# Kernel tuning notes

Measured on AMD Instinct MI355X. Metric: run time of the kernel, lower is better.

## Reference

```python
import jax, jax.numpy as jnp
import numpy as np

B = 64      # graphs per batch
N = 1024    # nodes per graph (equal-size graphs -> static top-k)
D = 256     # in_dim
DEG = 16    # avg degree
K = 512     # k = ratio * N, ratio = 0.5
E = B * N * DEG
NT = B * N


def setup_inputs() -> dict:
    key = jax.random.key(0)
    ks = jax.random.split(key, 8)
    feature = jax.random.normal(ks[0], (NT, D), jnp.float32)
    gid = jnp.repeat(jnp.arange(B), N * DEG)          # graph id per edge
    src = gid * N + jax.random.randint(ks[1], (E,), 0, N)
    dst = gid * N + jax.random.randint(ks[2], (E,), 0, N)
    label = jax.random.randint(ks[3], (B,), 0, 2)
    W = jax.random.normal(ks[4], (D, 1), jnp.float32) / np.sqrt(D)   # GraphConv weight
    b = jnp.zeros((1,), jnp.float32)                                  # GraphConv bias
    lin1_w = jax.random.normal(ks[5], (2, 1), jnp.float32) / np.sqrt(2.0)
    lin1_b = jnp.zeros((1,), jnp.float32)
    return dict(feature=feature, src=src, dst=dst, label=label,
                W=W, b=b, lin1_w=lin1_w, lin1_b=lin1_b)


def reference(feature, src, dst, label, W, b, lin1_w, lin1_b):
    fdt = feature.dtype
    # ---- get_bias_score: distance-to-class-center score ----
    node_label = jnp.repeat(label, N).astype(fdt)                 # [NT]
    gemb = feature.reshape(B, N, D).mean(axis=1)                  # AvgPooling per graph [B, D]
    lab_f = label.astype(fdt)                                     # [B]
    n1 = jnp.maximum(lab_f.sum(), 1.0)
    n0 = jnp.maximum((1.0 - lab_f).sum(), 1.0)
    center0 = (gemb * (1.0 - lab_f)[:, None]).sum(0) / n0         # [D]
    center1 = (gemb * lab_f[:, None]).sum(0) / n1                 # [D]
    d0 = jnp.sqrt(((feature - center0) ** 2).sum(-1))             # [NT]
    d1 = jnp.sqrt(((feature - center1) ** 2).sum(-1))             # [NT]
    score_distance = (d0 - d1) * ((node_label - 0.5) * 2.0)       # [NT]
    # ---- GraphConv(in_dim, 1), norm='both' (DGL semantics) ----
    ones_e = jnp.ones((E,), fdt)
    deg_out = jax.ops.segment_sum(ones_e, src, NT)
    deg_in = jax.ops.segment_sum(ones_e, dst, NT)
    ns = jnp.maximum(deg_out, 1.0) ** -0.5                        # src-side norm
    nd = jnp.maximum(deg_in, 1.0) ** -0.5                         # dst-side norm
    h = (feature @ W) * ns[:, None]                               # project first (out<in) [NT,1]
    agg = jax.ops.segment_sum(h[src], dst, NT)                    # [NT,1]
    score_gcn = (agg * nd[:, None] + b)[:, 0]                     # [NT]
    # ---- combine two scores with lin1: Linear(2, 1) ----
    score = jnp.stack([score_gcn, score_distance], axis=-1) @ lin1_w + lin1_b  # [NT,1]
    sflat = score[:, 0]
    # ---- per-graph top-k (mytopk with equal-size graphs -> static k) ----
    _, idx = jax.lax.top_k(sflat.reshape(B, N), K)                # [B,K] local indices
    perm = (idx + (jnp.arange(B) * N)[:, None]).reshape(-1)       # [B*K] global indices
    mask = jnp.ones((NT,), bool).at[perm].set(False)
    perm_com = jnp.nonzero(mask, size=NT - B * K)[0]              # complement, static size
    # ---- gather + tanh-gated features ----
    feature_dis = feature[perm] * jnp.tanh(sflat[perm])[:, None]          # [B*K, D]
    feature_com = feature[perm_com] * jnp.tanh(sflat[perm_com])[:, None]  # [B*(N-K), D]
    score_soft = jax.nn.softmax(score, axis=0)                    # softmax over all nodes
    return feature_dis, feature_com, perm, perm_com, score_soft
```

## Files before the change

### kernel.cpp

```cpp
#include <hip/hip_runtime.h>
#include <math.h>

#define Bg   64
#define Nn   1024
#define Dd   256
#define EPG  16384
#define NT   (Bg * Nn)
#define Kk   512

#define OFF_DIS   0
#define OFF_COM   8388608
#define OFF_PERM  16777216
#define OFF_PCOM  16809984
#define OFF_SOFT  16842752

#define WS_H0     0
#define WS_SFLAT  (NT * 4)
#define WS_GPART  (NT * 4 * 2)
#define WS_REDM   (WS_GPART + 1024 * 256 * 4)
#define WS_REDS   (WS_REDM + 256)
#define WS_C0     (WS_REDS + 256)
#define WS_C1     (WS_C0 + 1024)
#define WS_PERMI  (WS_C1 + 1024)
#define WS_PCOMI  (WS_PERMI + 32768 * 4)
#define WS_SGCN   (WS_PCOMI + 32768 * 4)

__global__ __launch_bounds__(256) void k_col(
        const float* __restrict__ f, const float* __restrict__ W,
        float* __restrict__ gpart, float* __restrict__ h0) {
    __shared__ float4 scol4[1024];
    int blk = blockIdx.x, t = threadIdx.x;
    int gid = t >> 4, sub = t & 15;
    int base = blk * 64 + gid * 4;
    const float4* f4 = (const float4*)f;
    const float4* W4 = (const float4*)W;
    float4 w[4];
    #pragma unroll
    for (int it = 0; it < 4; ++it) w[it] = W4[it * 16 + sub];
    float4 cs[4];
    #pragma unroll
    for (int it = 0; it < 4; ++it) cs[it] = make_float4(0.f, 0.f, 0.f, 0.f);
    float4 v[4][4];
    #pragma unroll
    for (int k = 0; k < 4; ++k) {
        size_t bofs = (size_t)(base + k) * 64;
        #pragma unroll
        for (int it = 0; it < 4; ++it) v[k][it] = f4[bofs + it * 16 + sub];
    }
    #pragma unroll
    for (int k = 0; k < 4; ++k) {
        float d = 0.f;
        #pragma unroll
        for (int it = 0; it < 4; ++it) {
            cs[it].x += v[k][it].x; cs[it].y += v[k][it].y;
            cs[it].z += v[k][it].z; cs[it].w += v[k][it].w;
            d += v[k][it].x * w[it].x + v[k][it].y * w[it].y
               + v[k][it].z * w[it].z + v[k][it].w * w[it].w;
        }
        #pragma unroll
        for (int o = 1; o < 16; o <<= 1) d += __shfl_xor(d, o);
        if (sub == 0) h0[base + k] = d;
    }
    #pragma unroll
    for (int it = 0; it < 4; ++it) scol4[gid * 64 + it * 16 + sub] = cs[it];
    __syncthreads();
    if (t < 64) {
        float4 s = make_float4(0.f, 0.f, 0.f, 0.f);
        #pragma unroll
        for (int g2 = 0; g2 < 16; ++g2) {
            float4 u = scol4[g2 * 64 + t];
            s.x += u.x; s.y += u.y; s.z += u.z; s.w += u.w;
        }
        ((float4*)(gpart + blk * Dd))[t] = s;
    }
}

__global__ __launch_bounds__(1024) void k_edge(
        const int* __restrict__ src, const int* __restrict__ dst,
        const int* __restrict__ label, const float* __restrict__ h0,
        const float* __restrict__ gpart, const float* __restrict__ b,
        float* __restrict__ sgcn, float* __restrict__ c0, float* __restrict__ c1) {
    __shared__ uint4 ep4[4096];
    __shared__ int   sdo[1024];
    __shared__ int   sdi[1024];
    __shared__ float shn[1024];
    __shared__ float ssc[1024];
    __shared__ float sc0[1024];
    __shared__ float sc1[1024];

    int g = blockIdx.x, t = threadIdx.x;
    sdo[t] = 0; sdi[t] = 0;

    if (g == 0) {
        int col = t & 255, chunk = t >> 8;
        float a0 = 0.f, a1 = 0.f;
        for (int gg = chunk * 16; gg < chunk * 16 + 16; ++gg) {
            float v = 0.f;
            #pragma unroll
            for (int p = 0; p < 16; ++p) v += gpart[(gg * 16 + p) * Dd + col];
            if (label[gg]) a1 += v; else a0 += v;
        }
        sc0[t] = a0; sc1[t] = a1;
        __syncthreads();
        if (t < Dd) {
            int n1 = 0;
            for (int gg = 0; gg < Bg; ++gg) n1 += label[gg];
            float fn1 = fmaxf((float)n1, 1.f);
            float fn0 = fmaxf((float)(Bg - n1), 1.f);
            float s0 = sc0[t] + sc0[256 + t] + sc0[512 + t] + sc0[768 + t];
            float s1 = sc1[t] + sc1[256 + t] + sc1[512 + t] + sc1[768 + t];
            c0[t] = s0 * (1.f / (float)Nn) / fn0;
            c1[t] = s1 * (1.f / (float)Nn) / fn1;
        }
    }
    __syncthreads();

    {
        const int4* s4 = (const int4*)(src + g * EPG);
        const int4* d4 = (const int4*)(dst + g * EPG);
        #pragma unroll
        for (int i = t; i < EPG / 4; i += 1024) {
            int4 ss = s4[i];
            int4 dd = d4[i];
            int s0 = ss.x & (Nn - 1), s1 = ss.y & (Nn - 1), s2 = ss.z & (Nn - 1), s3 = ss.w & (Nn - 1);
            int e0 = dd.x & (Nn - 1), e1 = dd.y & (Nn - 1), e2 = dd.z & (Nn - 1), e3 = dd.w & (Nn - 1);
            uint4 pk;
            pk.x = (unsigned)(s0 | (e0 << 16));
            pk.y = (unsigned)(s1 | (e1 << 16));
            pk.z = (unsigned)(s2 | (e2 << 16));
            pk.w = (unsigned)(s3 | (e3 << 16));
            ep4[i] = pk;
            atomicAdd(&sdo[s0], 1); atomicAdd(&sdo[s1], 1);
            atomicAdd(&sdo[s2], 1); atomicAdd(&sdo[s3], 1);
            atomicAdd(&sdi[e0], 1); atomicAdd(&sdi[e1], 1);
            atomicAdd(&sdi[e2], 1); atomicAdd(&sdi[e3], 1);
        }
    }
    __syncthreads();

    {
        int dg = sdo[t]; if (dg < 1) dg = 1;
        shn[t] = h0[g * Nn + t] / sqrtf((float)dg);
        ssc[t] = 0.f;
    }
    __syncthreads();

    #pragma unroll
    for (int i = t; i < EPG / 4; i += 1024) {
        uint4 pk = ep4[i];
        atomicAdd(&ssc[pk.x >> 16], shn[pk.x & 0xFFFF]);
        atomicAdd(&ssc[pk.y >> 16], shn[pk.y & 0xFFFF]);
        atomicAdd(&ssc[pk.z >> 16], shn[pk.z & 0xFFFF]);
        atomicAdd(&ssc[pk.w >> 16], shn[pk.w & 0xFFFF]);
    }
    __syncthreads();

    {
        int dg = sdi[t]; if (dg < 1) dg = 1;
        sgcn[g * Nn + t] = ssc[t] / sqrtf((float)dg) + b[0];
    }
}

__global__ __launch_bounds__(256) void k_score(
        const float* __restrict__ f, const float* __restrict__ c0,
        const float* __restrict__ c1, const float* __restrict__ sgcn,
        const int* __restrict__ label, const float* __restrict__ lw,
        const float* __restrict__ lb, float* __restrict__ sflat) {
    int t = threadIdx.x;
    int gid = t >> 4, sub = t & 15;
    int row0 = blockIdx.x * 32 + gid * 2;
    int g = row0 >> 10;
    const float4* f4 = (const float4*)f;
    float4 c0r[4], c1r[4];
    #pragma unroll
    for (int it = 0; it < 4; ++it) {
        c0r[it] = ((const float4*)c0)[it * 16 + sub];
        c1r[it] = ((const float4*)c1)[it * 16 + sub];
    }
    float sgn = label[g] ? 1.f : -1.f;
    float lw0 = lw[0], lw1 = lw[1], lb0 = lb[0];
    float4 v[2][4];
    #pragma unroll
    for (int r = 0; r < 2; ++r) {
        size_t bofs = (size_t)(row0 + r) * 64;
        #pragma unroll
        for (int it = 0; it < 4; ++it) v[r][it] = f4[bofs + it * 16 + sub];
    }
    #pragma unroll
    for (int r = 0; r < 2; ++r) {
        float a0 = 0.f, a1 = 0.f;
        #pragma unroll
        for (int it = 0; it < 4; ++it) {
            float dx;
            dx = v[r][it].x - c0r[it].x; a0 += dx * dx;
            dx = v[r][it].y - c0r[it].y; a0 += dx * dx;
            dx = v[r][it].z - c0r[it].z; a0 += dx * dx;
            dx = v[r][it].w - c0r[it].w; a0 += dx * dx;
            dx = v[r][it].x - c1r[it].x; a1 += dx * dx;
            dx = v[r][it].y - c1r[it].y; a1 += dx * dx;
            dx = v[r][it].z - c1r[it].z; a1 += dx * dx;
            dx = v[r][it].w - c1r[it].w; a1 += dx * dx;
        }
        #pragma unroll
        for (int o = 1; o < 16; o <<= 1) {
            a0 += __shfl_xor(a0, o);
            a1 += __shfl_xor(a1, o);
        }
        if (sub == 0) {
            int row = row0 + r;
            float sdist = (sqrtf(a0) - sqrtf(a1)) * sgn;
            sflat[row] = sgcn[row] * lw0 + sdist * lw1 + lb0;
        }
    }
}

__global__ __launch_bounds__(512) void k_topk(
        const float* __restrict__ sflat, int* __restrict__ permI,
        int* __restrict__ pcomI, float* __restrict__ out,
        float* __restrict__ redM, float* __restrict__ redS) {
    __shared__ unsigned long long sk[1024];
    __shared__ int   sflag[1024];
    __shared__ int   swave[8];
    __shared__ float sred[16];
    int g = blockIdx.x, t = threadIdx.x;
    int lane = t & 63, w = t >> 6;
    float v0 = sflat[g * Nn + t];
    float v1 = sflat[g * Nn + t + 512];
    unsigned u0 = __float_as_uint(v0);
    unsigned u1 = __float_as_uint(v1);
    unsigned o0 = u0 ^ ((u0 >> 31) ? 0xFFFFFFFFu : 0x80000000u);
    unsigned o1 = u1 ^ ((u1 >> 31) ? 0xFFFFFFFFu : 0x80000000u);
    sk[t]       = ((unsigned long long)o0 << 32) | (unsigned)(1023 - t);
    sk[t + 512] = ((unsigned long long)o1 << 32) | (unsigned)(1023 - (t + 512));
    __syncthreads();
    for (int k = 2; k <= 1024; k <<= 1) {
        for (int j = k >> 1; j > 0; j >>= 1) {
            int l = ((t & ~(j - 1)) << 1) | (t & (j - 1));
            int r = l | j;
            unsigned long long a = sk[l], bk = sk[r];
            bool up = ((l & k) == 0);
            if ((a < bk) == up) { sk[l] = bk; sk[r] = a; }
            __syncthreads();
        }
    }
    sflag[t] = 1; sflag[t + 512] = 1;
    __syncthreads();
    {
        int loc = 1023 - (int)(sk[t] & 0xFFFFFFFFu);
        sflag[loc] = 0;
        int gi = g * Nn + loc;
        permI[g * Kk + t] = gi;
        out[OFF_PERM + g * Kk + t] = (float)gi;
    }
    __syncthreads();
    int f0 = sflag[2 * t], f1 = sflag[2 * t + 1];
    int f2 = f0 + f1;
    int inc = f2;
    for (int o = 1; o < 64; o <<= 1) {
        int y = __shfl_up(inc, o);
        if (lane >= o) inc += y;
    }
    if (lane == 63) swave[w] = inc;
    __syncthreads();
    if (t < 8) {
        int a = swave[t];
        for (int o = 1; o < 8; o <<= 1) {
            int y = __shfl_up(a, o);
            if (t >= o) a += y;
        }
        swave[t] = a;
    }
    __syncthreads();
    int basep = ((w > 0) ? swave[w - 1] : 0) + (inc - f2);
    if (f0) {
        int gi = g * Nn + 2 * t;
        pcomI[g * Kk + basep] = gi;
        out[OFF_PCOM + g * Kk + basep] = (float)gi;
    }
    if (f1) {
        int pos = basep + f0;
        int gi = g * Nn + 2 * t + 1;
        pcomI[g * Kk + pos] = gi;
        out[OFF_PCOM + g * Kk + pos] = (float)gi;
    }
    float m = fmaxf(v0, v1);
    for (int o = 32; o > 0; o >>= 1) m = fmaxf(m, __shfl_xor(m, o));
    if (lane == 0) sred[w] = m;
    __syncthreads();
    if (t < 8) {
        float a = sred[t];
        for (int o = 4; o > 0; o >>= 1) a = fmaxf(a, __shfl_xor(a, o));
        if (t == 0) sred[0] = a;
    }
    __syncthreads();
    m = sred[0];
    float s = expf(v0 - m) + expf(v1 - m);
    for (int o = 32; o > 0; o >>= 1) s += __shfl_xor(s, o);
    if (lane == 0) sred[8 + w] = s;
    __syncthreads();
    if (t < 8) {
        float a = sred[8 + t];
        for (int o = 4; o > 0; o >>= 1) a += __shfl_xor(a, o);
        if (t == 0) { redM[g] = m; redS[g] = a; }
    }
}

__global__ __launch_bounds__(256) void k_write(
        const float* __restrict__ f, const int* __restrict__ permI,
        const int* __restrict__ pcomI, const float* __restrict__ sflat,
        const float* __restrict__ redM, const float* __restrict__ redS,
        float* __restrict__ out) {
    __shared__ float sMS[2];
    int t = threadIdx.x;
    if (t < 64) {
        float m = redM[t];
        float mm = m;
        for (int o = 32; o > 0; o >>= 1) mm = fmaxf(mm, __shfl_xor(mm, o));
        float s = redS[t] * expf(m - mm);
        for (int o = 32; o > 0; o >>= 1) s += __shfl_xor(s, o);
        if (t == 0) { sMS[0] = mm; sMS[1] = s; }
    }
    __syncthreads();
    float M = sMS[0], S = sMS[1];
    if (t < 32) {
        int i = blockIdx.x * 32 + t;
        out[OFF_SOFT + i] = expf(sflat[i] - M) / S;
    }
    int w = t >> 6, lane = t & 63;
    int j0 = blockIdx.x * 32 + w * 8;
    int rows[8];
    float tv[8];
    #pragma unroll
    for (int i = 0; i < 8; ++i) {
        int j = j0 + i;
        rows[i] = (j < 32768) ? permI[j] : pcomI[j - 32768];
    }
    #pragma unroll
    for (int i = 0; i < 8; ++i) tv[i] = sflat[rows[i]];
    #pragma unroll
    for (int i = 0; i < 8; ++i) tv[i] = tanhf(tv[i]);
    const float4* f4 = (const float4*)f;
    float4* o4 = (float4*)out;
    float4 v[8];
    #pragma unroll
    for (int i = 0; i < 8; ++i) v[i] = f4[(size_t)rows[i] * 64 + lane];
    #pragma unroll
    for (int i = 0; i < 8; ++i) {
        o4[(size_t)(j0 + i) * 64 + lane] =
            make_float4(v[i].x * tv[i], v[i].y * tv[i], v[i].z * tv[i], v[i].w * tv[i]);
    }
}

extern "C" void kernel_launch(void* const* d_in, const int* in_sizes, int n_in,
                              void* d_out, int out_size, void* d_ws, size_t ws_size,
                              hipStream_t stream) {
    const float* feature = (const float*)d_in[0];
    const int*   src     = (const int*)d_in[1];
    const int*   dst     = (const int*)d_in[2];
    const int*   label   = (const int*)d_in[3];
    const float* W       = (const float*)d_in[4];
    const float* b       = (const float*)d_in[5];
    const float* lw      = (const float*)d_in[6];
    const float* lb      = (const float*)d_in[7];
    float* out = (float*)d_out;
    char*  ws  = (char*)d_ws;

    float* h0    = (float*)(ws + WS_H0);
    float* sflat = (float*)(ws + WS_SFLAT);
    float* gpart = (float*)(ws + WS_GPART);
    float* redM  = (float*)(ws + WS_REDM);
    float* redS  = (float*)(ws + WS_REDS);
    float* c0    = (float*)(ws + WS_C0);
    float* c1    = (float*)(ws + WS_C1);
    int*   permI = (int*)(ws + WS_PERMI);
    int*   pcomI = (int*)(ws + WS_PCOMI);
    float* sgcn  = (float*)(ws + WS_SGCN);

    k_col  <<<1024, 256,  0, stream>>>(feature, W, gpart, h0);
    k_edge <<<Bg,   1024, 0, stream>>>(src, dst, label, h0, gpart, b, sgcn, c0, c1);
    k_score<<<2048, 256,  0, stream>>>(feature, c0, c1, sgcn, label, lw, lb, sflat);
    k_topk <<<Bg,   512,  0, stream>>>(sflat, permI, pcomI, out, redM, redS);
    k_write<<<2048, 256,  0, stream>>>(feature, permI, pcomI, sflat, redM, redS, out);
}
```

Before: 199.4 us.

## Overlap edge degree counting with feature column pass in one launch

The edge packing and degree histogram work now runs in 64 extra blocks of the feature column-sum/projection kernel, so it overlaps with the bandwidth-bound feature pass. The packed edges and degrees go to workspace, and a second kernel does only the scatter-add aggregation. The class-center reduction moves from block 0 into a separate 65th block, so it no longer serialises ahead of one graph's edge work. This adds global writes and reads of about 4 MB of packed edges and the degree arrays, and it uses 256-thread blocks for the histogram instead of 1024.

```diff
diff --git a/kernel.cpp b/kernel.cpp
--- a/kernel.cpp
+++ b/kernel.cpp
@@ -24,74 +24,133 @@
 #define WS_PERMI  (WS_C1 + 1024)
 #define WS_PCOMI  (WS_PERMI + 32768 * 4)
 #define WS_SGCN   (WS_PCOMI + 32768 * 4)
-
-__global__ __launch_bounds__(256) void k_col(
+#define WS_EPACK  (WS_SGCN + NT * 4)
+#define WS_DO     (WS_EPACK + Bg * EPG * 4)
+#define WS_DI     (WS_DO + NT * 4)
+
+__global__ __launch_bounds__(256) void k_mix(
         const float* __restrict__ f, const float* __restrict__ W,
-        float* __restrict__ gpart, float* __restrict__ h0) {
-    __shared__ float4 scol4[1024];
+        const int* __restrict__ src, const int* __restrict__ dst,
+        float* __restrict__ gpart, float* __restrict__ h0,
+        unsigned* __restrict__ epack, int* __restrict__ dout,
+        int* __restrict__ dinn) {
+    __shared__ alignas(16) char smem[16384];
     int blk = blockIdx.x, t = threadIdx.x;
-    int gid = t >> 4, sub = t & 15;
-    int base = blk * 64 + gid * 4;
-    const float4* f4 = (const float4*)f;
-    const float4* W4 = (const float4*)W;
-    float4 w[4];
-    #pragma unroll
-    for (int it = 0; it < 4; ++it) w[it] = W4[it * 16 + sub];
-    float4 cs[4];
-    #pragma unroll
-    for (int it = 0; it < 4; ++it) cs[it] = make_float4(0.f, 0.f, 0.f, 0.f);
-    float4 v[4][4];
-    #pragma unroll
-    for (int k = 0; k < 4; ++k) {
-        size_t bofs = (size_t)(base + k) * 64;
-        #pragma unroll
-        for (int it = 0; it < 4; ++it) v[k][it] = f4[bofs + it * 16 + sub];
-    }
-    #pragma unroll
-    for (int k = 0; k < 4; ++k) {
-        float d = 0.f;
-        #pragma unroll
-        for (int it = 0; it < 4; ++it) {
-            cs[it].x += v[k][it].x; cs[it].y += v[k][it].y;
-            cs[it].z += v[k][it].z; cs[it].w += v[k][it].w;
-            d += v[k][it].x * w[it].x + v[k][it].y * w[it].y
-               + v[k][it].z * w[it].z + v[k][it].w * w[it].w;
-        }
-        #pragma unroll
-        for (int o = 1; o < 16; o <<= 1) d += __shfl_xor(d, o);
-        if (sub == 0) h0[base + k] = d;
-    }
-    #pragma unroll
-    for (int it = 0; it < 4; ++it) scol4[gid * 64 + it * 16 + sub] = cs[it];
-    __syncthreads();
-    if (t < 64) {
-        float4 s = make_float4(0.f, 0.f, 0.f, 0.f);
-        #pragma unroll
-        for (int g2 = 0; g2 < 16; ++g2) {
-            float4 u = scol4[g2 * 64 + t];
-            s.x += u.x; s.y += u.y; s.z += u.z; s.w += u.w;
-        }
-        ((float4*)(gpart + blk * Dd))[t] = s;
-    }
-}
-
-__global__ __launch_bounds__(1024) void k_edge(
-        const int* __restrict__ src, const int* __restrict__ dst,
-        const int* __restrict__ label, const float* __restrict__ h0,
-        const float* __restrict__ gpart, const float* __restrict__ b,
-        float* __restrict__ sgcn, float* __restrict__ c0, float* __restrict__ c1) {
-    __shared__ uint4 ep4[4096];
-    __shared__ int   sdo[1024];
-    __shared__ int   sdi[1024];
+    if (blk < 1024) {
+        float4* scol4 = (float4*)smem;
+        int gid = t >> 4, sub = t & 15;
+        int base = blk * 64 + gid * 4;
+        const float4* f4 = (const float4*)f;
+        const float4* W4 = (const float4*)W;
+        float4 w[4];
+        #pragma unroll
+        for (int it = 0; it < 4; ++it) w[it] = W4[it * 16 + sub];
+        float4 cs[4];
+        #pragma unroll
+        for (int it = 0; it < 4; ++it) cs[it] = make_float4(0.f, 0.f, 0.f, 0.f);
+        float4 v[4][4];
+        #pragma unroll
+        for (int k = 0; k < 4; ++k) {
+            size_t bofs = (size_t)(base + k) * 64;
+            #pragma unroll
+            for (int it = 0; it < 4; ++it) v[k][it] = f4[bofs + it * 16 + sub];
+        }
+        #pragma unroll
+        for (int k = 0; k < 4; ++k) {
+            float d = 0.f;
+            #pragma unroll
+            for (int it = 0; it < 4; ++it) {
+                cs[it].x += v[k][it].x; cs[it].y += v[k][it].y;
+                cs[it].z += v[k][it].z; cs[it].w += v[k][it].w;
+                d += v[k][it].x * w[it].x + v[k][it].y * w[it].y
+                   + v[k][it].z * w[it].z + v[k][it].w * w[it].w;
+            }
+            #pragma unroll
+            for (int o = 1; o < 16; o <<= 1) d += __shfl_xor(d, o);
+            if (sub == 0) h0[base + k] = d;
+        }
+        #pragma unroll
+        for (int it = 0; it < 4; ++it) scol4[gid * 64 + it * 16 + sub] = cs[it];
+        __syncthreads();
+        if (t < 64) {
+            float4 s = make_float4(0.f, 0.f, 0.f, 0.f);
+            #pragma unroll
+            for (int g2 = 0; g2 < 16; ++g2) {
+                float4 u = scol4[g2 * 64 + t];
+                s.x += u.x; s.y += u.y; s.z += u.z; s.w += u.w;
+            }
+            ((float4*)(gpart + blk * Dd))[t] = s;
+        }
+    } else {
+        int* sdo = (int*)smem;
+        int* sdi = (int*)(smem + 4096);
+        int g = blk - 1024;
+        #pragma unroll
+        for (int j = 0; j < 4; ++j) { sdo[t + j * 256] = 0; sdi[t + j * 256] = 0; }
+        __syncthreads();
+        const int4* s4 = (const int4*)(src + g * EPG);
+        const int4* d4 = (const int4*)(dst + g * EPG);
+        uint4* p4 = (uint4*)(epack + g * EPG);
+        #pragma unroll
+        for (int i = t; i < EPG / 4; i += 256) {
+            int4 ss = s4[i];
+            int4 dd = d4[i];
+            int s0 = ss.x & (Nn - 1), s1 = ss.y & (Nn - 1), s2 = ss.z & (Nn - 1), s3 = ss.w & (Nn - 1);
+            int e0 = dd.x & (Nn - 1), e1 = dd.y & (Nn - 1), e2 = dd.z & (Nn - 1), e3 = dd.w & (Nn - 1);
+            uint4 pk;
+            pk.x = (unsigned)(s0 | (e0 << 16));
+            pk.y = (unsigned)(s1 | (e1 << 16));
+            pk.z = (unsigned)(s2 | (e2 << 16));
+            pk.w = (unsigned)(s3 | (e3 << 16));
+            p4[i] = pk;
+            atomicAdd(&sdo[s0], 1); atomicAdd(&sdo[s1], 1);
+            atomicAdd(&sdo[s2], 1); atomicAdd(&sdo[s3], 1);
+            atomicAdd(&sdi[e0], 1); atomicAdd(&sdi[e1], 1);
+            atomicAdd(&sdi[e2], 1); atomicAdd(&sdi[e3], 1);
+        }
+        __syncthreads();
+        #pragma unroll
+        for (int j = 0; j < 4; ++j) {
+            dout[g * Nn + t + j * 256] = sdo[t + j * 256];
+            dinn[g * Nn + t + j * 256] = sdi[t + j * 256];
+        }
+    }
+}
+
+__global__ __launch_bounds__(1024) void k_edge2(
+        const unsigned* __restrict__ epack, const int* __restrict__ dout,
+        const int* __restrict__ dinn, const int* __restrict__ label,
+        const float* __restrict__ h0, const float* __restrict__ gpart,
+        const float* __restrict__ b, float* __restrict__ sgcn,
+        float* __restrict__ c0, float* __restrict__ c1) {
     __shared__ float shn[1024];
     __shared__ float ssc[1024];
     __shared__ float sc0[1024];
     __shared__ float sc1[1024];
-
-    int g = blockIdx.x, t = threadIdx.x;
-    sdo[t] = 0; sdi[t] = 0;
-
-    if (g == 0) {
+    int blk = blockIdx.x, t = threadIdx.x;
+    if (blk < 64) {
+        int g = blk;
+        {
+            int dg = dout[g * Nn + t]; if (dg < 1) dg = 1;
+            shn[t] = h0[g * Nn + t] / sqrtf((float)dg);
+            ssc[t] = 0.f;
+        }
+        __syncthreads();
+        const uint4* p4 = (const uint4*)(epack + g * EPG);
+        #pragma unroll
+        for (int i = t; i < EPG / 4; i += 1024) {
+            uint4 pk = p4[i];
+            atomicAdd(&ssc[pk.x >> 16], shn[pk.x & 0xFFFF]);
+            atomicAdd(&ssc[pk.y >> 16], shn[pk.y & 0xFFFF]);
+            atomicAdd(&ssc[pk.z >> 16], shn[pk.z & 0xFFFF]);
+            atomicAdd(&ssc[pk.w >> 16], shn[pk.w & 0xFFFF]);
+        }
+        __syncthreads();
+        {
+            int dg = dinn[g * Nn + t]; if (dg < 1) dg = 1;
+            sgcn[g * Nn + t] = ssc[t] / sqrtf((float)dg) + b[0];
+        }
+    } else {
         int col = t & 255, chunk = t >> 8;
         float a0 = 0.f, a1 = 0.f;
         for (int gg = chunk * 16; gg < chunk * 16 + 16; ++gg) {
@@ -112,52 +171,6 @@
             c0[t] = s0 * (1.f / (float)Nn) / fn0;
             c1[t] = s1 * (1.f / (float)Nn) / fn1;
         }
-    }
-    __syncthreads();
-
-    {
-        const int4* s4 = (const int4*)(src + g * EPG);
-        const int4* d4 = (const int4*)(dst + g * EPG);
-        #pragma unroll
-        for (int i = t; i < EPG / 4; i += 1024) {
-            int4 ss = s4[i];
-            int4 dd = d4[i];
-            int s0 = ss.x & (Nn - 1), s1 = ss.y & (Nn - 1), s2 = ss.z & (Nn - 1), s3 = ss.w & (Nn - 1);
-            int e0 = dd.x & (Nn - 1), e1 = dd.y & (Nn - 1), e2 = dd.z & (Nn - 1), e3 = dd.w & (Nn - 1);
-            uint4 pk;
-            pk.x = (unsigned)(s0 | (e0 << 16));
-            pk.y = (unsigned)(s1 | (e1 << 16));
-            pk.z = (unsigned)(s2 | (e2 << 16));
-            pk.w = (unsigned)(s3 | (e3 << 16));
-            ep4[i] = pk;
-            atomicAdd(&sdo[s0], 1); atomicAdd(&sdo[s1], 1);
-            atomicAdd(&sdo[s2], 1); atomicAdd(&sdo[s3], 1);
-            atomicAdd(&sdi[e0], 1); atomicAdd(&sdi[e1], 1);
-            atomicAdd(&sdi[e2], 1); atomicAdd(&sdi[e3], 1);
-        }
-    }
-    __syncthreads();
-
-    {
-        int dg = sdo[t]; if (dg < 1) dg = 1;
-        shn[t] = h0[g * Nn + t] / sqrtf((float)dg);
-        ssc[t] = 0.f;
-    }
-    __syncthreads();
-
-    #pragma unroll
-    for (int i = t; i < EPG / 4; i += 1024) {
-        uint4 pk = ep4[i];
-        atomicAdd(&ssc[pk.x >> 16], shn[pk.x & 0xFFFF]);
-        atomicAdd(&ssc[pk.y >> 16], shn[pk.y & 0xFFFF]);
-        atomicAdd(&ssc[pk.z >> 16], shn[pk.z & 0xFFFF]);
-        atomicAdd(&ssc[pk.w >> 16], shn[pk.w & 0xFFFF]);
-    }
-    __syncthreads();
-
-    {
-        int dg = sdi[t]; if (dg < 1) dg = 1;
-        sgcn[g * Nn + t] = ssc[t] / sqrtf((float)dg) + b[0];
     }
 }
 
@@ -365,19 +378,22 @@
     float* out = (float*)d_out;
     char*  ws  = (char*)d_ws;
 
-    float* h0    = (float*)(ws + WS_H0);
-    float* sflat = (float*)(ws + WS_SFLAT);
-    float* gpart = (float*)(ws + WS_GPART);
-    float* redM  = (float*)(ws + WS_REDM);
-    float* redS  = (float*)(ws + WS_REDS);
-    float* c0    = (float*)(ws + WS_C0);
-    float* c1    = (float*)(ws + WS_C1);
-    int*   permI = (int*)(ws + WS_PERMI);
-    int*   pcomI = (int*)(ws + WS_PCOMI);
-    float* sgcn  = (float*)(ws + WS_SGCN);
-
-    k_col  <<<1024, 256,  0, stream>>>(feature, W, gpart, h0);
-    k_edge <<<Bg,   1024, 0, stream>>>(src, dst, label, h0, gpart, b, sgcn, c0, c1);
+    float*    h0    = (float*)(ws + WS_H0);
+    float*    sflat = (float*)(ws + WS_SFLAT);
+    float*    gpart = (float*)(ws + WS_GPART);
+    float*    redM  = (float*)(ws + WS_REDM);
+    float*    redS  = (float*)(ws + WS_REDS);
+    float*    c0    = (float*)(ws + WS_C0);
+    float*    c1    = (float*)(ws + WS_C1);
+    int*      permI = (int*)(ws + WS_PERMI);
+    int*      pcomI = (int*)(ws + WS_PCOMI);
+    float*    sgcn  = (float*)(ws + WS_SGCN);
+    unsigned* epack = (unsigned*)(ws + WS_EPACK);
+    int*      dout  = (int*)(ws + WS_DO);
+    int*      dinn  = (int*)(ws + WS_DI);
+
+    k_mix  <<<1088, 256,  0, stream>>>(feature, W, src, dst, gpart, h0, epack, dout, dinn);
+    k_edge2<<<65,   1024, 0, stream>>>(epack, dout, dinn, label, h0, gpart, b, sgcn, c0, c1);
     k_score<<<2048, 256,  0, stream>>>(feature, c0, c1, sgcn, label, lw, lb, sflat);
     k_topk <<<Bg,   512,  0, stream>>>(sflat, permI, pcomI, out, redM, redS);
     k_write<<<2048, 256,  0, stream>>>(feature, permI, pcomI, sflat, redM, redS, out);
```

Result: faster. 194.3 us (-2.6%).
